# Kernel tuning notes

Measured on AMD Instinct MI355X. Metric: run time of the kernel, lower is better.

## Reference

```python
import jax, jax.numpy as jnp
import numpy as np

T, B, H, W, CIN = 20, 16, 128, 128, 2
CH, OUT = 64, 10
BETA, THR = 0.9, 1.0


def spike(u):
    # Heaviside fire (surrogate grad only matters in bwd module)
    return (u > 0.0).astype(u.dtype)


def setup_inputs() -> dict:
    key = jax.random.key(0)
    k0, k1, k2 = jax.random.split(key, 3)
    x_seq = jax.random.normal(k0, (T, B, H, W, CIN), jnp.float32)
    w_conv = jax.random.normal(k1, (3, 3, CIN, CH), jnp.float32) * (1.0 / np.sqrt(9 * CIN))
    b_conv = jnp.zeros((CH,), jnp.float32)
    w_head = jax.random.normal(k2, (CH, OUT), jnp.float32) * (1.0 / np.sqrt(CH))
    b_head = jnp.zeros((OUT,), jnp.float32)
    return {"x_seq": x_seq, "w_conv": w_conv, "b_conv": b_conv,
            "w_head": w_head, "b_head": b_head}


def reference(x_seq, w_conv, b_conv, w_head, b_head):
    # temporal frame differences: [T-1, B, H, W, CIN]
    flow = x_seq[1:] - x_seq[:-1]
    t, b, h, w, c = flow.shape
    # conv is carry-independent: batch it over (time*batch) in one call
    u = jax.lax.conv_general_dilated(
        flow.reshape(t * b, h, w, c), w_conv,
        window_strides=(1, 1), padding='SAME',
        dimension_numbers=('NHWC', 'HWIO', 'NHWC')) + b_conv
    u = u.reshape(t, b, h, w, CH)  # [T-1, B, H, W, CH]

    def step(V, u_t):
        # LIF: leaky integrate, fire, soft reset
        V = BETA * V + u_t
        s = spike(V - THR)
        V = V - s * THR
        y = jnp.mean(s, axis=(1, 2)) @ w_head + b_head  # [B, OUT]
        return V, (y, jnp.mean(s))

    V0 = jnp.zeros((b, h, w, CH), u.dtype)
    _, (logits_seq, sr_seq) = jax.lax.scan(step, V0, u)
    readout = jnp.mean(logits_seq, axis=0)  # 'mean' readout
    return readout, logits_seq, jnp.asarray([jnp.mean(sr_seq)])
```

## Files before the change

kernel.cpp:

```cpp
#include <hip/hip_runtime.h>
#include <hip/hip_bf16.h>

#define TT   20
#define TS   19
#define BB   16
#define HH   128
#define WW   128
#define CINN 2
#define CHN  64
#define NOUT 10
#define BETA 0.9f
#define INVB (1.0f / BETA)

#define NCHUNK 5
#define NPB    128
#define SR_IDX (BB*NOUT + TS*BB*NOUT)

#define PPD      132
#define ROWB     (PPD*4)
#define PROWS    129
#define PLANE_B  (PROWS*ROWB)
#define FRAME_B  (2*PLANE_B)
#define FLOW_B   ((size_t)BB*TS*FRAME_B)
#define SLACK_B  528
#define CNT_OFF4 ((size_t)(FLOW_B + SLACK_B) / 4)
#define CNT_B    ((size_t)BB*NCHUNK*NPB*CHN*4)
#define WS_NEED  (FLOW_B + SLACK_B + CNT_B)

#define LROW  20

typedef __attribute__((ext_vector_type(8))) short short8;
typedef __attribute__((ext_vector_type(4))) float float4v;
typedef __attribute__((ext_vector_type(4))) int   int4v;
typedef unsigned uint4v_t __attribute__((ext_vector_type(4)));
typedef uint4v_t __attribute__((aligned(4))) uint4vu;

__device__ __forceinline__ unsigned rne16(float f) {
    unsigned u = __float_as_uint(f);
    return (u + 0x7fffu + ((u >> 16) & 1u)) >> 16;
}
__device__ __forceinline__ float b2f(unsigned us) { return __uint_as_float(us << 16); }
__device__ __forceinline__ unsigned rndb(float f) {
    unsigned u = __float_as_uint(f);
    return u + 0x7fffu + ((u >> 16) & 1u);
}
__device__ __forceinline__ void pack2(float d0, float d1, unsigned &hi, unsigned &lo) {
    unsigned r0 = rndb(d0), r1 = rndb(d1);
    hi = __builtin_amdgcn_perm(r1, r0, 0x07060302u);
    float e0 = d0 - __uint_as_float(r0 & 0xffff0000u);
    float e1 = d1 - __uint_as_float(r1 & 0xffff0000u);
    lo = __builtin_amdgcn_perm(rndb(e1), rndb(e0), 0x07060302u);
}

__global__ __launch_bounds__(256) void flow_pack(const float* __restrict__ x,
                                                 unsigned* __restrict__ wsf) {
    const int t = blockIdx.x;
    const int b = blockIdx.y;
    const int z = blockIdx.z;
    const int tid = threadIdx.x;

    float ct = 1.f;
    for (int i = 0; i < t; ++i) ct *= INVB;

    const float2* x0 = (const float2*)x + ((size_t)t * BB + b) * (HH * WW);
    const float2* x1 = x0 + (size_t)BB * HH * WW;
    char* fb = (char*)wsf + ((size_t)b * TS + t) * FRAME_B;

#pragma unroll
    for (int i = 0; i < 8; ++i) {
        int p  = i * 256 + tid;
        int y  = (z << 4) + (p >> 7);
        int px = p & 127;
        float2 a = x1[y * WW + px], c = x0[y * WW + px];
        float d0 = (a.x - c.x) * ct, d1 = (a.y - c.y) * ct;
        unsigned hw, lw; pack2(d0, d1, hw, lw);
        unsigned off = (unsigned)(y * PPD + px + 1) * 4u;
        *(unsigned*)(fb + off) = hw;
        *(unsigned*)(fb + PLANE_B + off) = lw;
    }
    if (tid < 128) {
        int y  = (z << 4) + (tid >> 3);
        int c  = tid & 7;
        int pl = c >> 2;
        int pp = (c & 3) == 0 ? 0 : 128 + (c & 3);
        *(unsigned*)(fb + pl * PLANE_B + (y * PPD + pp) * 4) = 0u;
    }
    if (z == 0) {
        for (int d = tid; d < 2 * PPD; d += 256) {
            int pl = d / PPD, pp = d - pl * PPD;
            *(unsigned*)(fb + pl * PLANE_B + (128 * PPD + pp) * 4) = 0u;
        }
        if (t == 0 && b == 0 && tid < PPD)
            *((unsigned*)((char*)wsf + FLOW_B) + tid) = 0u;
    }
}

__global__ __launch_bounds__(256, 4) void lif_fast(const char* __restrict__ flow,
                                                   const float* __restrict__ w_conv,
                                                   const float* __restrict__ b_conv,
                                                   int* __restrict__ cw,
                                                   float* __restrict__ out) {
    __shared__ int lds_cnt[NCHUNK][CHN];

    const int tid  = threadIdx.x;
    const int lane = tid & 63;
    const int wv   = __builtin_amdgcn_readfirstlane(tid >> 6);
    const int bx   = blockIdx.x;
    const int r0   = blockIdx.y << 1;
    const int bz   = blockIdx.z;
    const int q    = lane >> 4;
    const int col  = lane & 15;
    const int x0   = (bx << 6) + (wv << 4);
    const int qsh  = q << 3;

    if (bx == 0 && blockIdx.y == 0 && bz == 0) {
        if (tid < BB * NOUT) out[tid] = 0.f;
        else if (tid == BB * NOUT) out[SR_IDX] = 0.f;
    }
    if (tid < NCHUNK * CHN - 256) ((int*)lds_cnt)[256 + tid] = 0;
    ((int*)lds_cnt)[tid] = 0;
    __syncthreads();

    const int rq  = (q < 3) ? q : 0;
    const int yA0 = r0 - 1 + rq, yA1 = yA0 + 1;
    const int ym0 = ((unsigned)yA0 < (unsigned)HH) ? yA0 : 128;
    const int ym1 = ((unsigned)yA1 < (unsigned)HH) ? yA1 : 128;
    const unsigned offH0 = (unsigned)(ym0 * ROWB + (x0 + col) * 4);
    const unsigned offH1 = (unsigned)(ym1 * ROWB + (x0 + col) * 4);

    short8 Bh[4], Bl[4];
#pragma unroll
    for (int cg = 0; cg < 4; ++cg) {
        int hi_i[4] = {0, 0, 0, 0}, lo_i[4] = {0, 0, 0, 0};
        if (q < 3) {
#pragma unroll
            for (int j = 0; j < 6; ++j) {
                float w = w_conv[((q * 3 + (j >> 1)) * 2 + (j & 1)) * CHN + cg * 16 + col];
                unsigned hs = rne16(w);
                unsigned ls = rne16(w - b2f(hs));
                hi_i[j >> 1] |= (int)(hs << (16 * (j & 1)));
                lo_i[j >> 1] |= (int)(ls << (16 * (j & 1)));
            }
        }
        int4v hv = {hi_i[0], hi_i[1], hi_i[2], hi_i[3]};
        int4v lv = {lo_i[0], lo_i[1], lo_i[2], lo_i[3]};
        Bh[cg] = __builtin_bit_cast(short8, hv);
        Bl[cg] = __builtin_bit_cast(short8, lv);
    }

    float nb[4];
#pragma unroll
    for (int cg = 0; cg < 4; ++cg) nb[cg] = -b_conv[cg * 16 + col];

    float4v W0[4], W1[4];
#pragma unroll
    for (int cg = 0; cg < 4; ++cg) {
        W0[cg] = (float4v){0.f, 0.f, 0.f, 0.f};
        W1[cg] = (float4v){0.f, 0.f, 0.f, 0.f};
    }

    float ct = 1.0f, S = 1.0f;
    int pendA = 0, pendB = 0;
    unsigned cur = 0;

    const char* fp = flow + (size_t)bz * TS * FRAME_B;
    uint4vu eH0 = *(const uint4vu*)(fp + offH0);
    uint4vu eH1 = *(const uint4vu*)(fp + offH1);
    uint4vu eL0 = *(const uint4vu*)(fp + PLANE_B + offH0);
    uint4vu eL1 = *(const uint4vu*)(fp + PLANE_B + offH1);
    fp += FRAME_B;
    uint4vu oH0, oH1, oL0, oL1;

#define STEP(T_, CH0, CH1, CL0, CL1, NH0, NH1, NL0, NL1, DPOS, DODEF, DOFLUSH, CK, DOLOAD) do { \
    int cp1_ = 0, sh2_ = 0;                                                     \
    if (DODEF) { cp1_ = pendA + pendB; sh2_ = __shfl_xor(cp1_, 32); }           \
    if (DOLOAD) {                                                               \
        NH0 = *(const uint4vu*)(fp + offH0);                                    \
        NH1 = *(const uint4vu*)(fp + offH1);                                    \
        NL0 = *(const uint4vu*)(fp + PLANE_B + offH0);                          \
        NL1 = *(const uint4vu*)(fp + PLANE_B + offH1);                          \
        fp += FRAME_B;                                                          \
    }                                                                           \
    float ctn = ct * INVB;                                                      \
    short8 A0h = __builtin_bit_cast(short8, CH0);                               \
    short8 A1h = __builtin_bit_cast(short8, CH1);                               \
    short8 A0l = __builtin_bit_cast(short8, CL0);                               \
    short8 A1l = __builtin_bit_cast(short8, CL1);                               \
    __builtin_amdgcn_s_setprio(1);                                              \
    _Pragma("unroll")                                                           \
    for (int cg = 0; cg < 4; ++cg) {                                            \
        W0[cg] = __builtin_amdgcn_mfma_f32_16x16x32_bf16(A0h, Bh[cg], W0[cg], 0, 0, 0); \
        W1[cg] = __builtin_amdgcn_mfma_f32_16x16x32_bf16(A1h, Bh[cg], W1[cg], 0, 0, 0); \
    }                                                                           \
    _Pragma("unroll")                                                           \
    for (int cg = 0; cg < 4; ++cg) {                                            \
        W0[cg] = __builtin_amdgcn_mfma_f32_16x16x32_bf16(A0l, Bh[cg], W0[cg], 0, 0, 0); \
        W1[cg] = __builtin_amdgcn_mfma_f32_16x16x32_bf16(A1l, Bh[cg], W1[cg], 0, 0, 0); \
    }                                                                           \
    _Pragma("unroll")                                                           \
    for (int cg = 0; cg < 4; ++cg) {                                            \
        W0[cg] = __builtin_amdgcn_mfma_f32_16x16x32_bf16(A0h, Bl[cg], W0[cg], 0, 0, 0); \
        W1[cg] = __builtin_amdgcn_mfma_f32_16x16x32_bf16(A1h, Bl[cg], W1[cg], 0, 0, 0); \
    }                                                                           \
    __builtin_amdgcn_s_setprio(0);                                              \
    if (DODEF) {                                                                \
        unsigned cnt_ = ((unsigned)(cp1_ + sh2_) >> qsh) & 255u;                \
        cur |= cnt_ << (8 * (DPOS));                                            \
        if (DOFLUSH) { atomicAdd(&lds_cnt[CK][lane], (int)cur); cur = 0u; }     \
    }                                                                           \
    int cpack = 0;                                                              \
    _Pragma("unroll")                                                           \
    for (int cg = 0; cg < 4; ++cg) {                                            \
        float thr = fmaf(nb[cg], S, ct);                                        \
        float4v w0 = W0[cg], w1 = W1[cg];                                       \
        int c = 0;                                                              \
        _Pragma("unroll")                                                       \
        for (int r = 0; r < 4; ++r) {                                           \
            float v0 = w0[r]; bool s0 = v0 > thr;                               \
            w0[r] = s0 ? (v0 - ct) : v0; c += s0;                               \
            float v1 = w1[r]; bool s1 = v1 > thr;                               \
            w1[r] = s1 ? (v1 - ct) : v1; c += s1;                               \
        }                                                                       \
        W0[cg] = w0; W1[cg] = w1;                                               \
        cpack |= c << (8 * cg);                                                 \
    }                                                                           \
    pendA = cpack;                                                              \
    pendB = __shfl_xor(cpack, 16);                                              \
    ct = ctn; S += ctn;                                                         \
} while (0)

#pragma unroll 1
    for (int c = 0; c < 4; ++c) {
        STEP(4 * c + 0, eH0, eH1, eL0, eL1, oH0, oH1, oL0, oL1, 3, (c > 0), (c > 0), (c - 1), 1);
        STEP(4 * c + 1, oH0, oH1, oL0, oL1, eH0, eH1, eL0, eL1, 0, 1, 0, 0, 1);
        STEP(4 * c + 2, eH0, eH1, eL0, eL1, oH0, oH1, oL0, oL1, 1, 1, 0, 0, 1);
        STEP(4 * c + 3, oH0, oH1, oL0, oL1, eH0, eH1, eL0, eL1, 2, 1, 0, 0, 1);
    }
    STEP(16, eH0, eH1, eL0, eL1, oH0, oH1, oL0, oL1, 3, 1, 1, 3, 1);
    STEP(17, oH0, oH1, oL0, oL1, eH0, eH1, eL0, eL1, 0, 1, 0, 0, 1);
    STEP(18, eH0, eH1, eL0, eL1, oH0, oH1, oL0, oL1, 1, 1, 0, 0, 0);
#undef STEP

    {
        int cp1 = pendA + pendB;
        int cp2 = cp1 + __shfl_xor(cp1, 32);
        unsigned cnt = ((unsigned)cp2 >> qsh) & 255u;
        cur |= cnt << 16;
        atomicAdd(&lds_cnt[4][lane], (int)cur);
    }
    __syncthreads();

    {
        const int pb = (blockIdx.y << 1) | bx;
        const int k0 = tid >> 6, ch = tid & 63;
        cw[((bz * NCHUNK + k0) * NPB + pb) * CHN + ch] = lds_cnt[k0][ch];
        if (tid < CHN)
            cw[((bz * NCHUNK + 4) * NPB + pb) * CHN + tid] = lds_cnt[4][tid];
    }
}

__global__ __launch_bounds__(256, 4) void lif_main(const float* __restrict__ x,
                                                   const float* __restrict__ w_conv,
                                                   const float* __restrict__ b_conv,
                                                   int* __restrict__ ws,
                                                   float* __restrict__ out) {
    __shared__ unsigned lds[4][2][2][4 * LROW];
    __shared__ int lds_cnt[NCHUNK][CHN];

    const float2* xp2 = (const float2*)x;
    const int FRAME2  = BB * HH * WW;

    const int tid  = threadIdx.x;
    const int lane = tid & 63;
    const int wv   = __builtin_amdgcn_readfirstlane(tid >> 6);
    const int bx   = blockIdx.x;
    const int r0   = blockIdx.y << 1;
    const int bz   = blockIdx.z;
    const int q    = lane >> 4;
    const int col  = lane & 15;
    const int x0   = (bx << 6) + (wv << 4);
    const int qsh  = q << 3;

    if (bx == 0 && blockIdx.y == 0 && bz == 0) {
        if (tid < BB * NOUT) out[tid] = 0.f;
        else if (tid == BB * NOUT) out[SR_IDX] = 0.f;
    }
    if (tid < NCHUNK * CHN - 256) ((int*)lds_cnt)[256 + tid] = 0;
    ((int*)lds_cnt)[tid] = 0;
    __syncthreads();

    const int  row0 = lane / 18, dx0 = lane - row0 * 18;
    const int  y0s  = r0 - 1 + row0;
    const int  px0s = x0 - 1 + dx0;
    const bool val0 = ((unsigned)y0s < (unsigned)HH) && ((unsigned)px0s < (unsigned)WW);
    const int  off0 = val0 ? (y0s * WW + px0s) : 0;
    const int  ls0  = row0 * LROW + dx0;

    const bool act1 = (lane < 8);
    const int  y1s  = r0 + 2;
    const int  px1s = x0 - 1 + 10 + lane;
    const bool val1 = act1 && ((unsigned)y1s < (unsigned)HH) && ((unsigned)px1s < (unsigned)WW);
    const int  off1 = val1 ? (y1s * WW + px1s) : 0;
    const int  ls1  = 3 * LROW + 10 + lane;

    const int rq  = (q < 3) ? q : 0;
    const int rdb = rq * LROW + col;

    short8 Bh[4], Bl[4];
#pragma unroll
    for (int cg = 0; cg < 4; ++cg) {
        int hi_i[4] = {0, 0, 0, 0}, lo_i[4] = {0, 0, 0, 0};
        if (q < 3) {
#pragma unroll
            for (int j = 0; j < 6; ++j) {
                float w = w_conv[((q * 3 + (j >> 1)) * 2 + (j & 1)) * CHN + cg * 16 + col];
                unsigned hs = rne16(w);
                unsigned ls = rne16(w - b2f(hs));
                hi_i[j >> 1] |= (int)(hs << (16 * (j & 1)));
                lo_i[j >> 1] |= (int)(ls << (16 * (j & 1)));
            }
        }
        int4v hv = {hi_i[0], hi_i[1], hi_i[2], hi_i[3]};
        int4v lv = {lo_i[0], lo_i[1], lo_i[2], lo_i[3]};
        Bh[cg] = __builtin_bit_cast(short8, hv);
        Bl[cg] = __builtin_bit_cast(short8, lv);
    }

    float nb[4];
#pragma unroll
    for (int cg = 0; cg < 4; ++cg) nb[cg] = -b_conv[cg * 16 + col];

    float4v W0[4], W1[4];
#pragma unroll
    for (int cg = 0; cg < 4; ++cg) {
        W0[cg] = (float4v){0.f, 0.f, 0.f, 0.f};
        W1[cg] = (float4v){0.f, 0.f, 0.f, 0.f};
    }

    float ct = 1.0f, S = 1.0f;
    int pendA = 0, pendB = 0;
    unsigned cur = 0;

    float2 ra_0 = {0.f, 0.f}, rb_0 = {0.f, 0.f}, rc_0 = {0.f, 0.f};
    float2 ra_1 = {0.f, 0.f}, rb_1 = {0.f, 0.f}, rc_1 = {0.f, 0.f};
    const float2* xb = xp2 + bz * HH * WW;
    if (val0) { rb_0 = xb[off0]; ra_0 = xb[FRAME2 + off0]; rc_0 = xb[2 * FRAME2 + off0]; }
    if (val1) { rb_1 = xb[off1]; ra_1 = xb[FRAME2 + off1]; rc_1 = xb[2 * FRAME2 + off1]; }
    {
        unsigned* hiW = &lds[wv][0][0][0];
        unsigned* loW = &lds[wv][0][1][0];
        {
            float d0 = (ra_0.x - rb_0.x), d1 = (ra_0.y - rb_0.y);
            unsigned hw, lw; pack2(d0, d1, hw, lw);
            hiW[ls0] = hw; loW[ls0] = lw;
        }
        if (act1) {
            float d0 = (ra_1.x - rb_1.x), d1 = (ra_1.y - rb_1.y);
            unsigned hw, lw; pack2(d0, d1, hw, lw);
            hiW[ls1] = hw; loW[ls1] = lw;
        }
        rb_0 = ra_0; ra_0 = rc_0;
        rb_1 = ra_1; ra_1 = rc_1;
        if (val0) rc_0 = xb[3 * FRAME2 + off0];
        if (val1) rc_1 = xb[3 * FRAME2 + off1];
    }
    const float2* xn = xb + 4 * FRAME2;

#define STEP(T_, CURB, NXTB, DPOS, DODEF, DOFLUSH, CK, DOSTAGE, DOPREF) do {    \
    const unsigned* hiR = &lds[wv][CURB][0][0] + rdb;                           \
    const unsigned* loR = &lds[wv][CURB][1][0] + rdb;                           \
    unsigned h0 = hiR[0], h1 = hiR[1], h2 = hiR[2];                             \
    unsigned h3 = hiR[LROW], h4 = hiR[LROW + 1], h5 = hiR[LROW + 2];            \
    unsigned l0 = loR[0], l1 = loR[1], l2 = loR[2];                             \
    unsigned l3 = loR[LROW], l4 = loR[LROW + 1], l5 = loR[LROW + 2];            \
    int cp1_ = 0, sh2_ = 0;                                                     \
    if (DODEF) { cp1_ = pendA + pendB; sh2_ = __shfl_xor(cp1_, 32); }           \
    float ctn = ct * INVB;                                                      \
    if (DOSTAGE) {                                                              \
        unsigned* hiW = &lds[wv][NXTB][0][0];                                   \
        unsigned* loW = &lds[wv][NXTB][1][0];                                   \
        {                                                                       \
            float d0 = (ra_0.x - rb_0.x) * ctn;                                 \
            float d1 = (ra_0.y - rb_0.y) * ctn;                                 \
            unsigned hw, lw; pack2(d0, d1, hw, lw);                             \
            hiW[ls0] = hw; loW[ls0] = lw;                                       \
        }                                                                       \
        if (act1) {                                                             \
            float d0 = (ra_1.x - rb_1.x) * ctn;                                 \
            float d1 = (ra_1.y - rb_1.y) * ctn;                                 \
            unsigned hw, lw; pack2(d0, d1, hw, lw);                             \
            hiW[ls1] = hw; loW[ls1] = lw;                                       \
        }                                                                       \
        rb_0 = ra_0; ra_0 = rc_0;                                               \
        rb_1 = ra_1; ra_1 = rc_1;                                               \
        if (DOPREF) {                                                           \
            if (val0) rc_0 = xn[off0];                                          \
            if (val1) rc_1 = xn[off1];                                          \
            xn += FRAME2;                                                       \
        }                                                                       \
    }                                                                           \
    int4v a0h = {(int)h0, (int)h1, (int)h2, (int)h0};                           \
    int4v a0l = {(int)l0, (int)l1, (int)l2, (int)l0};                           \
    int4v a1h = {(int)h3, (int)h4, (int)h5, (int)h3};                           \
    int4v a1l = {(int)l3, (int)l4, (int)l5, (int)l3};                           \
    short8 A0h = __builtin_bit_cast(short8, a0h);                               \
    short8 A0l = __builtin_bit_cast(short8, a0l);                               \
    short8 A1h = __builtin_bit_cast(short8, a1h);                               \
    short8 A1l = __builtin_bit_cast(short8, a1l);                               \
    __builtin_amdgcn_s_setprio(1);                                              \
    _Pragma("unroll")                                                           \
    for (int cg = 0; cg < 4; ++cg) {                                            \
        W0[cg] = __builtin_amdgcn_mfma_f32_16x16x32_bf16(A0h, Bh[cg], W0[cg], 0, 0, 0); \
        W1[cg] = __builtin_amdgcn_mfma_f32_16x16x32_bf16(A1h, Bh[cg], W1[cg], 0, 0, 0); \
    }                                                                           \
    _Pragma("unroll")                                                           \
    for (int cg = 0; cg < 4; ++cg) {                                            \
        W0[cg] = __builtin_amdgcn_mfma_f32_16x16x32_bf16(A0l, Bh[cg], W0[cg], 0, 0, 0); \
        W1[cg] = __builtin_amdgcn_mfma_f32_16x16x32_bf16(A1l, Bh[cg], W1[cg], 0, 0, 0); \
    }                                                                           \
    _Pragma("unroll")                                                           \
    for (int cg = 0; cg < 4; ++cg) {                                            \
        W0[cg] = __builtin_amdgcn_mfma_f32_16x16x32_bf16(A0h, Bl[cg], W0[cg], 0, 0, 0); \
        W1[cg] = __builtin_amdgcn_mfma_f32_16x16x32_bf16(A1h, Bl[cg], W1[cg], 0, 0, 0); \
    }                                                                           \
    __builtin_amdgcn_s_setprio(0);                                              \
    if (DODEF) {                                                                \
        unsigned cnt_ = ((unsigned)(cp1_ + sh2_) >> qsh) & 255u;                \
        cur |= cnt_ << (8 * (DPOS));                                            \
        if (DOFLUSH) { atomicAdd(&lds_cnt[CK][lane], (int)cur); cur = 0u; }     \
    }                                                                           \
    int cpack = 0;                                                              \
    _Pragma("unroll")                                                           \
    for (int cg = 0; cg < 4; ++cg) {                                            \
        float thr = fmaf(nb[cg], S, ct);                                        \
        float4v w0 = W0[cg], w1 = W1[cg];                                       \
        int c = 0;                                                              \
        _Pragma("unroll")                                                       \
        for (int r = 0; r < 4; ++r) {                                           \
            float v0 = w0[r]; bool s0 = v0 > thr;                               \
            w0[r] = s0 ? (v0 - ct) : v0; c += s0;                               \
            float v1 = w1[r]; bool s1 = v1 > thr;                               \
            w1[r] = s1 ? (v1 - ct) : v1; c += s1;                               \
        }                                                                       \
        W0[cg] = w0; W1[cg] = w1;                                               \
        cpack |= c << (8 * cg);                                                 \
    }                                                                           \
    pendA = cpack;                                                              \
    pendB = __shfl_xor(cpack, 16);                                              \
    ct = ctn; S += ctn;                                                         \
} while (0)

#pragma unroll 1
    for (int c = 0; c < 4; ++c) {
        STEP(4 * c + 0, 0, 1, 3, (c > 0), (c > 0), (c - 1), 1, 1);
        STEP(4 * c + 1, 1, 0, 0, 1, 0, 0, 1, 1);
        STEP(4 * c + 2, 0, 1, 1, 1, 0, 0, 1, 1);
        STEP(4 * c + 3, 1, 0, 2, 1, 0, 0, 1, 1);
    }
    STEP(16, 0, 1, 3, 1, 1, 3, 1, 0);
    STEP(17, 1, 0, 0, 1, 0, 0, 1, 0);
    STEP(18, 0, 1, 1, 1, 0, 0, 0, 0);
#undef STEP

    {
        int cp1 = pendA + pendB;
        int cp2 = cp1 + __shfl_xor(cp1, 32);
        unsigned cnt = ((unsigned)cp2 >> qsh) & 255u;
        cur |= cnt << 16;
        atomicAdd(&lds_cnt[4][lane], (int)cur);
    }
    __syncthreads();

    {
        const int pb = (blockIdx.y << 1) | bx;
        const int k0 = tid >> 6, ch = tid & 63;
        ws[((bz * NCHUNK + k0) * NPB + pb) * CHN + ch] = lds_cnt[k0][ch];
        if (tid < CHN)
            ws[((bz * NCHUNK + 4) * NPB + pb) * CHN + tid] = lds_cnt[4][tid];
    }
}

__global__ __launch_bounds__(64) void head_kernel(const int* __restrict__ cw,
                                                  const float* __restrict__ w_head,
                                                  const float* __restrict__ b_head,
                                                  float* __restrict__ out) {
    const int t = blockIdx.x, b = blockIdx.y, ch = threadIdx.x;
    const int k = t >> 2, sh = (t & 3) << 3;
    const int* base = cw + ((b * NCHUNK + k) * NPB) * CHN + ch;

    int cnt = 0;
#pragma unroll 8
    for (int p = 0; p < NPB; ++p) cnt += (base[p * CHN] >> sh) & 255;

    const float s = (float)cnt * (1.f / (HH * WW));
    float acc[NOUT];
#pragma unroll
    for (int o = 0; o < NOUT; ++o) acc[o] = s * w_head[ch * NOUT + o];
    float tt = (float)cnt;
#pragma unroll
    for (int off = 32; off > 0; off >>= 1) {
#pragma unroll
        for (int o = 0; o < NOUT; ++o) acc[o] += __shfl_down(acc[o], off);
        tt += __shfl_down(tt, off);
    }
    if (ch == 0) {
#pragma unroll
        for (int o = 0; o < NOUT; ++o) {
            float lg = acc[o] + b_head[o];
            out[BB * NOUT + (t * BB + b) * NOUT + o] = lg;
            atomicAdd(&out[b * NOUT + o], lg * (1.f / TS));
        }
        atomicAdd(&out[SR_IDX], tt * (1.f / ((float)TS * BB * HH * WW * CHN)));
    }
}

extern "C" void kernel_launch(void* const* d_in, const int* in_sizes, int n_in,
                              void* d_out, int out_size, void* d_ws, size_t ws_size,
                              hipStream_t stream) {
    (void)in_sizes; (void)n_in; (void)out_size;
    const float* x      = (const float*)d_in[0];
    const float* w_conv = (const float*)d_in[1];
    const float* b_conv = (const float*)d_in[2];
    const float* w_head = (const float*)d_in[3];
    const float* b_head = (const float*)d_in[4];
    float* out = (float*)d_out;

    if (ws_size >= WS_NEED) {
        unsigned* wsf = (unsigned*)d_ws;
        int* cw = (int*)d_ws + CNT_OFF4;
        flow_pack<<<dim3(TS, BB, 8), 256, 0, stream>>>(x, wsf);
        lif_fast<<<dim3(2, HH / 2, BB), 256, 0, stream>>>((const char*)d_ws, w_conv, b_conv, cw, out);
        head_kernel<<<dim3(TS, BB), 64, 0, stream>>>(cw, w_head, b_head, out);
    } else {
        int* cw = (int*)d_ws;
        lif_main<<<dim3(2, HH / 2, BB), 256, 0, stream>>>(x, w_conv, b_conv, cw, out);
        head_kernel<<<dim3(TS, BB), 64, 0, stream>>>(cw, w_head, b_head, out);
    }
}
```

Before: 171.6 us.

## Stream flow_pack over time per pixel to reuse frames and widen loads

flow_pack now gives each thread two pixels and loops over all time steps. It carries the previous frame in registers so every input frame is read once instead of twice, and it uses float4 loads and 8-byte stores. The grid shrinks from (19,16,8) to (32,16), which lowers parallelism but roughly halves input traffic. lif_fast's launch bound is also loosened from 4 to 3 waves per SIMD, which gives it more registers at the cost of occupancy.

```diff
diff --git a/kernel.cpp b/kernel.cpp
--- a/kernel.cpp
+++ b/kernel.cpp
@@ -34,6 +34,8 @@
 typedef __attribute__((ext_vector_type(4))) int   int4v;
 typedef unsigned uint4v_t __attribute__((ext_vector_type(4)));
 typedef uint4v_t __attribute__((aligned(4))) uint4vu;
+typedef unsigned uint2v_t __attribute__((ext_vector_type(2)));
+typedef uint2v_t __attribute__((aligned(4))) uint2vu;
 
 __device__ __forceinline__ unsigned rne16(float f) {
     unsigned u = __float_as_uint(f);
@@ -54,48 +56,52 @@
 
 __global__ __launch_bounds__(256) void flow_pack(const float* __restrict__ x,
                                                  unsigned* __restrict__ wsf) {
-    const int t = blockIdx.x;
-    const int b = blockIdx.y;
-    const int z = blockIdx.z;
+    const int bx  = blockIdx.x;
+    const int b   = blockIdx.y;
     const int tid = threadIdx.x;
-
+    const int row = (bx << 2) + (tid >> 6);
+    const int p0  = (tid & 63) << 1;
+
+    const int TSTR = BB * HH * WW / 2;
+    const float4* xr = (const float4*)x + ((b * HH + row) * WW + p0) / 2;
+    char* fb = (char*)wsf + (size_t)b * TS * FRAME_B;
+    const unsigned off = (unsigned)(row * PPD + p0 + 1) * 4u;
+
+    float4 cur = xr[0];
+    float4 nxt = xr[TSTR];
     float ct = 1.f;
-    for (int i = 0; i < t; ++i) ct *= INVB;
-
-    const float2* x0 = (const float2*)x + ((size_t)t * BB + b) * (HH * WW);
-    const float2* x1 = x0 + (size_t)BB * HH * WW;
-    char* fb = (char*)wsf + ((size_t)b * TS + t) * FRAME_B;
-
-#pragma unroll
-    for (int i = 0; i < 8; ++i) {
-        int p  = i * 256 + tid;
-        int y  = (z << 4) + (p >> 7);
-        int px = p & 127;
-        float2 a = x1[y * WW + px], c = x0[y * WW + px];
-        float d0 = (a.x - c.x) * ct, d1 = (a.y - c.y) * ct;
-        unsigned hw, lw; pack2(d0, d1, hw, lw);
-        unsigned off = (unsigned)(y * PPD + px + 1) * 4u;
-        *(unsigned*)(fb + off) = hw;
-        *(unsigned*)(fb + PLANE_B + off) = lw;
-    }
-    if (tid < 128) {
-        int y  = (z << 4) + (tid >> 3);
-        int c  = tid & 7;
-        int pl = c >> 2;
-        int pp = (c & 3) == 0 ? 0 : 128 + (c & 3);
-        *(unsigned*)(fb + pl * PLANE_B + (y * PPD + pp) * 4) = 0u;
-    }
-    if (z == 0) {
-        for (int d = tid; d < 2 * PPD; d += 256) {
-            int pl = d / PPD, pp = d - pl * PPD;
-            *(unsigned*)(fb + pl * PLANE_B + (128 * PPD + pp) * 4) = 0u;
-        }
-        if (t == 0 && b == 0 && tid < PPD)
-            *((unsigned*)((char*)wsf + FLOW_B) + tid) = 0u;
-    }
-}
-
-__global__ __launch_bounds__(256, 4) void lif_fast(const char* __restrict__ flow,
+#pragma unroll 1
+    for (int t = 0; t < TS; ++t) {
+        float4 fut = nxt;
+        if (t + 2 <= TS) fut = xr[(t + 2) * TSTR];
+        float d0 = (nxt.x - cur.x) * ct, d1 = (nxt.y - cur.y) * ct;
+        float d2 = (nxt.z - cur.z) * ct, d3 = (nxt.w - cur.w) * ct;
+        unsigned h0, l0, h1, l1;
+        pack2(d0, d1, h0, l0);
+        pack2(d2, d3, h1, l1);
+        uint2v_t hv = {h0, h1}, lv = {l0, l1};
+        *(uint2vu*)(fb + off) = hv;
+        *(uint2vu*)(fb + PLANE_B + off) = lv;
+        if ((tid & 63) < 8) {
+            int c  = tid & 7;
+            int pl = c >> 2;
+            int pp = (c & 3) == 0 ? 0 : 128 + (c & 3);
+            *(unsigned*)(fb + pl * PLANE_B + (row * PPD + pp) * 4) = 0u;
+        }
+        if (bx == 0) {
+            for (int d = tid; d < 2 * PPD; d += 256) {
+                int pl = d >= PPD, pp = d - pl * PPD;
+                *(unsigned*)(fb + pl * PLANE_B + (128 * PPD + pp) * 4) = 0u;
+            }
+        }
+        cur = nxt; nxt = fut;
+        fb += FRAME_B; ct *= INVB;
+    }
+    if (bx == 0 && b == 0 && tid < PPD)
+        *((unsigned*)((char*)wsf + FLOW_B) + tid) = 0u;
+}
+
+__global__ __launch_bounds__(256, 3) void lif_fast(const char* __restrict__ flow,
                                                    const float* __restrict__ w_conv,
                                                    const float* __restrict__ b_conv,
                                                    int* __restrict__ cw,
@@ -528,7 +534,7 @@
     if (ws_size >= WS_NEED) {
         unsigned* wsf = (unsigned*)d_ws;
         int* cw = (int*)d_ws + CNT_OFF4;
-        flow_pack<<<dim3(TS, BB, 8), 256, 0, stream>>>(x, wsf);
+        flow_pack<<<dim3(32, BB), 256, 0, stream>>>(x, wsf);
         lif_fast<<<dim3(2, HH / 2, BB), 256, 0, stream>>>((const char*)d_ws, w_conv, b_conv, cw, out);
         head_kernel<<<dim3(TS, BB), 64, 0, stream>>>(cw, w_head, b_head, out);
     } else {
```

Result: faster. 167.4 us (-2.5%).
